# Performance work log

Measured on AMD Instinct MI355X. Metric: run time of the kernel, lower is better.

Reference implementation:

```python
import jax, jax.numpy as jnp
import numpy as np
from jax import lax

B, C, OUT, K, H, W = 8, 64, 32, 3, 64, 64


def _conv2d(x, w, b, stride=1, pad=0, groups=1):
    o = lax.conv_general_dilated(x, w, (stride, stride), [(pad, pad), (pad, pad)],
                                 dimension_numbers=('NCHW', 'OIHW', 'NCHW'),
                                 feature_group_count=groups)
    return o + b[None, :, None, None]


def _bn(x, g, b, m, v, eps=1e-5):
    # eval-mode BatchNorm2d with running stats
    s = g / jnp.sqrt(v + eps)
    return x * s[None, :, None, None] + (b - m * s)[None, :, None, None]


def _eca(x, w):
    # global avg pool -> 1D conv over channel axis -> sigmoid gate [b,c,1,1]
    y = x.mean((-2, -1))[:, None, :]  # [b,1,c]
    y = lax.conv_general_dilated(y, w, (1,), [(1, 1)],
                                 dimension_numbers=('NCW', 'OIW', 'NCW'))
    return jax.nn.sigmoid(y[:, 0, :])[:, :, None, None]


def _avgpool3(x):
    # AvgPool2d(k=3, stride=1, pad=1), count_include_pad=True (torch default)
    s = lax.reduce_window(x, 0.0, lax.add, (1, 1, 3, 3), (1, 1, 1, 1),
                          [(0, 0), (0, 0), (1, 1), (1, 1)])
    return s / 9.0


def _forward(x, sc_w, sc_b, ac_w, ac_b, oc_w, oc_b, oc_bn_g, oc_bn_b, oc_bn_m, oc_bn_v,
             ex_w, ey_w, ez_w, ff_w, ff_b, g1_w, g1_b, g2_w, g2_b,
             fu_w, fu_b, fu_bn_g, fu_bn_b, fu_bn_m, fu_bn_v):
    b, c, h, w = x.shape
    k = K
    # --- ReceptiveFieldAttentionConv ---
    frf = jax.nn.silu(_conv2d(x, sc_w, sc_b, pad=k // 2, groups=c))
    frf = frf.reshape(b, c, k * k, h, w)
    arf = _conv2d(_avgpool3(x), ac_w, ac_b, groups=c).reshape(b, c, k * k, h, w)
    arf = jax.nn.softmax(arf, axis=2)  # softmax over k*k RF positions
    wt = (frf * arf).reshape(b, c, k, k, h, w)
    wt = wt.transpose(0, 1, 4, 2, 5, 3).reshape(b, c, h * k, w * k)  # pixel-shuffle-like
    x_rfa = jax.nn.silu(_bn(_conv2d(wt, oc_w, oc_b, stride=k, groups=4),
                            oc_bn_g, oc_bn_b, oc_bn_m, oc_bn_v))
    # --- FrequencyGroupedChannelAttention ---
    energy = jnp.abs(jnp.fft.fft2(x)).mean((-2, -1))  # [b,c]
    ranks = jnp.argsort(jnp.argsort(-energy, axis=1), axis=1)
    mask = (ranks < c // 2).astype(x.dtype)[:, :, None, None]  # top-half-energy channels
    a_x = _eca(x, ex_w)
    a_y = _eca(x * mask, ey_w)
    a_z = _eca(x * (1.0 - mask), ez_w)
    a_f = _conv2d(jnp.concatenate([a_y, a_z], 1), ff_w, ff_b, groups=4)
    g_in = jnp.concatenate([a_f, a_x], 1)
    g = jax.nn.sigmoid(_conv2d(jax.nn.silu(_conv2d(g_in, g1_w, g1_b)), g2_w, g2_b))
    x_fgca = x * (g * a_f + (1.0 - g) * a_x)
    # --- fuse ---
    fused = jnp.concatenate([x_rfa, x_fgca], 1)
    return jax.nn.silu(_bn(_conv2d(fused, fu_w, fu_b),
                           fu_bn_g, fu_bn_b, fu_bn_m, fu_bn_v))


def setup_inputs() -> dict:
    key = jax.random.key(0)
    ks = jax.random.split(key, 32)
    rn = lambda k, shp, s=0.1: jax.random.normal(k, shp, jnp.float32) * s
    gh = max(8, C // 4)  # gate hidden = 16
    return {
        'x': jax.random.normal(ks[0], (B, C, H, W), jnp.float32),
        'sc_w': rn(ks[1], (C * K * K, 1, K, K)), 'sc_b': rn(ks[2], (C * K * K,)),
        'ac_w': rn(ks[3], (C * K * K, 1, 1, 1)), 'ac_b': rn(ks[4], (C * K * K,)),
        'oc_w': rn(ks[5], (C, C // 4, K, K)), 'oc_b': rn(ks[6], (C,)),
        'oc_bn_g': 1.0 + rn(ks[7], (C,)), 'oc_bn_b': rn(ks[8], (C,)),
        'oc_bn_m': rn(ks[9], (C,)), 'oc_bn_v': 0.9 + 0.2 * jax.random.uniform(ks[10], (C,), jnp.float32),
        'ex_w': rn(ks[11], (1, 1, 3), 0.3), 'ey_w': rn(ks[12], (1, 1, 3), 0.3),
        'ez_w': rn(ks[13], (1, 1, 3), 0.3),
        'ff_w': rn(ks[14], (C, 2 * C // 4, 1, 1)), 'ff_b': rn(ks[15], (C,)),
        'g1_w': rn(ks[16], (gh, 2 * C, 1, 1)), 'g1_b': rn(ks[17], (gh,)),
        'g2_w': rn(ks[18], (C, gh, 1, 1)), 'g2_b': rn(ks[19], (C,)),
        'fu_w': rn(ks[20], (OUT, 2 * C, 1, 1)), 'fu_b': rn(ks[21], (OUT,)),
        'fu_bn_g': 1.0 + rn(ks[22], (OUT,)), 'fu_bn_b': rn(ks[23], (OUT,)),
        'fu_bn_m': rn(ks[24], (OUT,)), 'fu_bn_v': 0.9 + 0.2 * jax.random.uniform(ks[25], (OUT,), jnp.float32),
    }


def reference(x, sc_w, sc_b, ac_w, ac_b, oc_w, oc_b, oc_bn_g, oc_bn_b, oc_bn_m, oc_bn_v,
              ex_w, ey_w, ez_w, ff_w, ff_b, g1_w, g1_b, g2_w, g2_b,
              fu_w, fu_b, fu_bn_g, fu_bn_b, fu_bn_m, fu_bn_v):
    return _forward(x, sc_w, sc_b, ac_w, ac_b, oc_w, oc_b, oc_bn_g, oc_bn_b, oc_bn_m, oc_bn_v,
                    ex_w, ey_w, ez_w, ff_w, ff_b, g1_w, g1_b, g2_w, g2_b,
                    fu_w, fu_b, fu_bn_g, fu_bn_b, fu_bn_m, fu_bn_v)
```

## Files before the change

kernel.cpp:

```cpp
#include <hip/hip_runtime.h>
#include <math.h>

#define EPS 1e-5f

__device__ __forceinline__ float wave_sum(float v) {
  v += __shfl_down(v, 32);
  v += __shfl_down(v, 16);
  v += __shfl_down(v, 8);
  v += __shfl_down(v, 4);
  v += __shfl_down(v, 2);
  v += __shfl_down(v, 1);
  return v;
}

__device__ __forceinline__ float frcp(float x) { return __builtin_amdgcn_rcpf(x); }
__device__ __forceinline__ float silu_f(float v) { return v * frcp(1.f + __expf(-v)); }
__device__ __forceinline__ float sigm_f(float v) { return frcp(1.f + __expf(-v)); }

__device__ __forceinline__ unsigned bf16r(float v) {
  unsigned u = __float_as_uint(v);
  return (u + 0x7FFFu + ((u >> 16) & 1u)) >> 16;
}

__device__ __forceinline__ int bitrev6(int v) {
  return ((v & 1) << 5) | ((v & 2) << 3) | ((v & 4) << 1) |
         ((v & 8) >> 1) | ((v & 16) >> 3) | ((v & 32) >> 5);
}

#define FFT6(zr, zi)                                           \
  do {                                                         \
    _Pragma("unroll") for (int s = 0; s < 6; ++s) {            \
      const int half = 32 >> s;                                \
      const bool up = (lane & half) != 0;                      \
      float pr = __shfl_xor(zr, half);                         \
      float pi = __shfl_xor(zi, half);                         \
      float tr = up ? pr - zr : zr + pr;                       \
      float ti = up ? pi - zi : zi + pi;                       \
      const float c = twc[s], sn = tws[s];                     \
      zr = tr * c - ti * sn;                                   \
      zi = tr * sn + ti * c;                                   \
    }                                                          \
  } while (0)

__global__ __launch_bounds__(256) void k_dft(const float* __restrict__ x,
                                             float* __restrict__ energy,
                                             float* __restrict__ meanx) {
  __shared__ float re1[33 * 65];
  __shared__ float im1[33 * 65];
  __shared__ float redA[4], redB[4];
  const int bc = blockIdx.x;
  const int tid = threadIdx.x;
  const int lane = tid & 63;
  const int wv = tid >> 6;
  const float* xp = x + (size_t)bc * 4096;

  float twc[6], tws[6];
#pragma unroll
  for (int s = 0; s < 6; ++s) {
    int half = 32 >> s;
    if (lane & half) {
      float ang = -6.283185307179586f * (float)((lane & (half - 1)) << s) / 64.f;
      float sv, cv;
      __sincosf(ang, &sv, &cv);
      twc[s] = cv;
      tws[s] = sv;
    } else {
      twc[s] = 1.f;
      tws[s] = 0.f;
    }
  }

  const int f = bitrev6(lane);
  const int fm = (64 - f) & 63;
  const int plane = bitrev6(fm);

  float lsum = 0.f;
#pragma unroll 1
  for (int rp = 0; rp < 4; ++rp) {
    const int h0 = wv * 16 + rp * 4;
    float x0 = xp[h0 * 64 + lane];
    float x1 = xp[(h0 + 1) * 64 + lane];
    float x2 = xp[(h0 + 2) * 64 + lane];
    float x3 = xp[(h0 + 3) * 64 + lane];
    lsum += x0 + x1 + x2 + x3;
    float zr = x0, zi = x1, yr = x2, yi = x3;
#pragma unroll
    for (int s = 0; s < 6; ++s) {
      const int half = 32 >> s;
      const bool up = (lane & half) != 0;
      float pzr = __shfl_xor(zr, half);
      float pzi = __shfl_xor(zi, half);
      float pyr = __shfl_xor(yr, half);
      float pyi = __shfl_xor(yi, half);
      float tzr = up ? pzr - zr : zr + pzr;
      float tzi = up ? pzi - zi : zi + pzi;
      float tyr = up ? pyr - yr : yr + pyr;
      float tyi = up ? pyi - yi : yi + pyi;
      const float c = twc[s], sn = tws[s];
      zr = tzr * c - tzi * sn;
      zi = tzr * sn + tzi * c;
      yr = tyr * c - tyi * sn;
      yi = tyr * sn + tyi * c;
    }
    float mzr = __shfl(zr, plane), mzi = __shfl(zi, plane);
    float myr = __shfl(yr, plane), myi = __shfl(yi, plane);
    if (f <= 32) {
      float ar = 0.5f * (zr + mzr), ai = 0.5f * (zi - mzi);
      float br = 0.5f * (zi + mzi), bi = 0.5f * (mzr - zr);
      float cr = 0.5f * (yr + myr), ci = 0.5f * (yi - myi);
      float dr = 0.5f * (yi + myi), di = 0.5f * (myr - yr);
      re1[f * 65 + h0] = ar;     im1[f * 65 + h0] = ai;
      re1[f * 65 + h0 + 1] = br; im1[f * 65 + h0 + 1] = bi;
      re1[f * 65 + h0 + 2] = cr; im1[f * 65 + h0 + 2] = ci;
      re1[f * 65 + h0 + 3] = dr; im1[f * 65 + h0 + 3] = di;
    }
  }
  __syncthreads();

  float msum = 0.f;
#pragma unroll 1
  for (int i = 0; i < 4; ++i) {
    const int kv1 = wv + 8 * i;
    const int kv2 = kv1 + 4;
    const float w1 = (kv1 == 0) ? 1.f : 2.f;
    float ar = re1[kv1 * 65 + lane];
    float ai = im1[kv1 * 65 + lane];
    float br = re1[kv2 * 65 + lane];
    float bi = im1[kv2 * 65 + lane];
#pragma unroll
    for (int s = 0; s < 6; ++s) {
      const int half = 32 >> s;
      const bool up = (lane & half) != 0;
      float par = __shfl_xor(ar, half);
      float pai = __shfl_xor(ai, half);
      float pbr = __shfl_xor(br, half);
      float pbi = __shfl_xor(bi, half);
      float tar = up ? par - ar : ar + par;
      float tai = up ? pai - ai : ai + pai;
      float tbr = up ? pbr - br : br + pbr;
      float tbi = up ? pbi - bi : bi + pbi;
      const float c = twc[s], sn = tws[s];
      ar = tar * c - tai * sn;
      ai = tar * sn + tai * c;
      br = tbr * c - tbi * sn;
      bi = tbr * sn + tbi * c;
    }
    msum += w1 * sqrtf(ar * ar + ai * ai) + 2.f * sqrtf(br * br + bi * bi);
  }
  if (wv == 0) {
    float ar = re1[32 * 65 + lane];
    float ai = im1[32 * 65 + lane];
    FFT6(ar, ai);
    msum += sqrtf(ar * ar + ai * ai);
  }

  msum = wave_sum(msum);
  lsum = wave_sum(lsum);
  if (lane == 0) { redA[wv] = msum; redB[wv] = lsum; }
  __syncthreads();
  if (tid == 0) {
    float e = redA[0] + redA[1] + redA[2] + redA[3];
    float m = redB[0] + redB[1] + redB[2] + redB[3];
    energy[bc] = e * (1.f / 4096.f);
    meanx[bc] = m * (1.f / 4096.f);
  }
}

__global__ __launch_bounds__(256) void k_rfa(
    const float* __restrict__ x,
    const float* __restrict__ sc_w, const float* __restrict__ sc_b,
    const float* __restrict__ ac_w, const float* __restrict__ ac_b,
    const float* __restrict__ oc_w, const float* __restrict__ oc_b,
    const float* __restrict__ bn_g, const float* __restrict__ bn_b,
    const float* __restrict__ bn_m, const float* __restrict__ bn_v,
    float* __restrict__ xrfa) {
  __shared__ __align__(16) float scwp[16 * 9 * 12];
  __shared__ __align__(16) float mp[16 * 24];
  __shared__ __align__(16) unsigned ocwb[16 * 8 * 12];
  __shared__ float red[128 * 33];
  const int blk = blockIdx.x;
  const int band = blk & 15;
  const int g = (blk >> 4) & 3;
  const int b = blk >> 6;
  const int tid = threadIdx.x;
  const int lane = tid & 63;
  const int wv = tid >> 6;
  const int wp = wv & 1;
  const int half = wv >> 1;

  for (int i = tid; i < 1296; i += 256) {
    int icg = i / 81, rem = i - icg * 81;
    int j = rem / 9, t = rem - j * 9;
    scwp[icg * 108 + j * 12 + t] = sc_w[(g * 144 + icg * 9 + j) * 9 + t];
  }
  if (tid < 144) {
    int icg = tid / 9, j = tid - icg * 9;
    scwp[icg * 108 + j * 12 + 9] = sc_b[g * 144 + tid];
    mp[icg * 24 + j] = ac_w[g * 144 + tid];
    mp[icg * 24 + 12 + j] = ac_b[g * 144 + tid];
  }
  for (int i = tid; i < 1152; i += 256) {
    int icg = i / 72, rem = i - icg * 72;
    int o2 = rem / 9, j = rem - o2 * 9;
    float w0 = oc_w[((g * 16 + 2 * o2) * 16 + icg) * 9 + j];
    float w1 = oc_w[((g * 16 + 2 * o2 + 1) * 16 + icg) * 9 + j];
    ocwb[icg * 96 + o2 * 12 + j] = bf16r(w0) | (bf16r(w1) << 16);
  }
  __syncthreads();

  const int r0 = band * 4 + wp * 2;
  const int w = lane;
  const bool vW = w > 0, vE = w < 63;
  float acc0[16], acc1[16];
#pragma unroll
  for (int i = 0; i < 16; ++i) { acc0[i] = 0.f; acc1[i] = 0.f; }

  const float* xg = x + ((size_t)(b * 64 + g * 16)) * 4096 + w;
  const int icg0 = half * 8;

#pragma unroll 1
  for (int ii = 0; ii < 8; ++ii) {
    const int icg = icg0 + ii;
    const float* xc = xg + icg * 4096;
    float n[12];
#pragma unroll
    for (int t = 0; t < 4; ++t) {
      int h = r0 - 1 + t;
      bool vh = (h >= 0) && (h < 64);
      const float* row = xc + h * 64;
      n[t * 3 + 0] = (vh && vW) ? row[-1] : 0.f;
      n[t * 3 + 1] = vh ? row[0] : 0.f;
      n[t * 3 + 2] = (vh && vE) ? row[1] : 0.f;
    }
    float rs0 = n[0] + n[1] + n[2];
    float rs1 = n[3] + n[4] + n[5];
    float rs2 = n[6] + n[7] + n[8];
    float rs3 = n[9] + n[10] + n[11];
    float ap0 = (rs0 + rs1 + rs2) * (1.f / 9.f);
    float ap1 = (rs1 + rs2 + rs3) * (1.f / 9.f);

    float aw[12], ab[12];
    *(float4*)&aw[0] = *(const float4*)&mp[icg * 24];
    *(float4*)&aw[4] = *(const float4*)&mp[icg * 24 + 4];
    *(float4*)&aw[8] = *(const float4*)&mp[icg * 24 + 8];
    *(float4*)&ab[0] = *(const float4*)&mp[icg * 24 + 12];
    *(float4*)&ab[4] = *(const float4*)&mp[icg * 24 + 16];
    *(float4*)&ab[8] = *(const float4*)&mp[icg * 24 + 20];

    float f0[9], f1[9], a0[9], a1[9];
    float amax0 = -1e30f, amax1 = -1e30f;
#pragma unroll
    for (int j = 0; j < 9; ++j) {
      float wt[12];
      *(float4*)&wt[0] = *(const float4*)&scwp[icg * 108 + j * 12];
      *(float4*)&wt[4] = *(const float4*)&scwp[icg * 108 + j * 12 + 4];
      *(float4*)&wt[8] = *(const float4*)&scwp[icg * 108 + j * 12 + 8];
      float p0 = wt[9], p1 = wt[9];
#pragma unroll
      for (int t = 0; t < 9; ++t) {
        p0 = fmaf(n[t], wt[t], p0);
        p1 = fmaf(n[t + 3], wt[t], p1);
      }
      f0[j] = silu_f(p0);
      f1[j] = silu_f(p1);
      float v0 = fmaf(ap0, aw[j], ab[j]);
      float v1 = fmaf(ap1, aw[j], ab[j]);
      a0[j] = v0; a1[j] = v1;
      amax0 = fmaxf(amax0, v0);
      amax1 = fmaxf(amax1, v1);
    }
    float es0 = 0.f, es1 = 0.f;
    float p0[9], p1[9];
#pragma unroll
    for (int j = 0; j < 9; ++j) {
      float e0 = __expf(a0[j] - amax0);
      float e1 = __expf(a1[j] - amax1);
      es0 += e0; es1 += e1;
      p0[j] = f0[j] * e0;
      p1[j] = f1[j] * e1;
    }
    float i0 = frcp(es0);
    float i1 = frcp(es1);
#pragma unroll
    for (int j = 0; j < 9; ++j) { p0[j] *= i0; p1[j] *= i1; }

#pragma unroll
    for (int o2 = 0; o2 < 8; ++o2) {
      unsigned u[12];
      *(uint4*)&u[0] = *(const uint4*)&ocwb[icg * 96 + o2 * 12];
      *(uint4*)&u[4] = *(const uint4*)&ocwb[icg * 96 + o2 * 12 + 4];
      *(uint4*)&u[8] = *(const uint4*)&ocwb[icg * 96 + o2 * 12 + 8];
      float se0 = 0.f, so0 = 0.f, se1 = 0.f, so1 = 0.f;
#pragma unroll
      for (int j = 0; j < 9; ++j) {
        float we = __uint_as_float(u[j] << 16);
        float wo = __uint_as_float(u[j] & 0xFFFF0000u);
        se0 = fmaf(p0[j], we, se0);
        so0 = fmaf(p0[j], wo, so0);
        se1 = fmaf(p1[j], we, se1);
        so1 = fmaf(p1[j], wo, so1);
      }
      acc0[2 * o2] += se0;
      acc0[2 * o2 + 1] += so0;
      acc1[2 * o2] += se1;
      acc1[2 * o2 + 1] += so1;
    }
  }

  const int rid = wp * 64 + lane;
  if (half == 1) {
#pragma unroll
    for (int k = 0; k < 16; ++k) {
      red[rid * 33 + k] = acc0[k];
      red[rid * 33 + 16 + k] = acc1[k];
    }
  }
  __syncthreads();
  if (half == 0) {
#pragma unroll
    for (int k = 0; k < 16; ++k) {
      acc0[k] += red[rid * 33 + k];
      acc1[k] += red[rid * 33 + 16 + k];
    }
    float* op = xrfa + ((size_t)(b * 64 + g * 16)) * 4096 + r0 * 64 + w;
#pragma unroll
    for (int oco = 0; oco < 16; ++oco) {
      int oc = g * 16 + oco;
      float s = bn_g[oc] * rsqrtf(bn_v[oc] + EPS);
      float bb = bn_b[oc] - bn_m[oc] * s;
      float ob = oc_b[oc];
      float v0 = fmaf(acc0[oco] + ob, s, bb);
      float v1 = fmaf(acc1[oco] + ob, s, bb);
      op[oco * 4096] = silu_f(v0);
      op[oco * 4096 + 64] = silu_f(v1);
    }
  }
}

__global__ __launch_bounds__(256) void k_fuse(
    const float* __restrict__ x, const float* __restrict__ xrfa,
    const float* __restrict__ energy, const float* __restrict__ meanx,
    const float* __restrict__ ex_w, const float* __restrict__ ey_w,
    const float* __restrict__ ez_w, const float* __restrict__ ff_w,
    const float* __restrict__ ff_b, const float* __restrict__ g1_w,
    const float* __restrict__ g1_b, const float* __restrict__ g2_w,
    const float* __restrict__ g2_b,
    const float* __restrict__ fu_w, const float* __restrict__ fu_b,
    const float* __restrict__ bn_g, const float* __restrict__ bn_b,
    const float* __restrict__ bn_m, const float* __restrict__ bn_v,
    float* __restrict__ out) {
  __shared__ __align__(16) float fw[4096];
  __shared__ float s2l[64];
  __shared__ float e[64], mx[64], my[64], mz[64];
  __shared__ float ax[64], ay[64], az[64], af[64], h1[16];
  const int blk = blockIdx.x;
  const int tid = threadIdx.x;
  const int sloc = tid & 63;
  const int ocq = tid >> 6;
  const int b = blk >> 6;
  const int sp = (blk & 63) * 64 + sloc;
  const int c = tid;

  for (int i = tid; i < 1024; i += 256)
    ((float4*)fw)[i] = ((const float4*)fu_w)[i];
  if (c < 64) {
    e[c] = energy[b * 64 + c];
    mx[c] = meanx[b * 64 + c];
  }
  __syncthreads();
  if (c < 64) {
    int rank = 0;
    float ec = e[c];
    for (int i = 0; i < 64; ++i) {
      float ei = e[i];
      rank += (ei > ec) || (ei == ec && i < c);
    }
    float mask = (rank < 32) ? 1.f : 0.f;
    my[c] = mx[c] * mask;
    mz[c] = mx[c] * (1.f - mask);
  }
  __syncthreads();
  if (c < 64) {
    float l, r, m;
    l = (c > 0) ? mx[c - 1] : 0.f; m = mx[c]; r = (c < 63) ? mx[c + 1] : 0.f;
    ax[c] = sigm_f(ex_w[0] * l + ex_w[1] * m + ex_w[2] * r);
    l = (c > 0) ? my[c - 1] : 0.f; m = my[c]; r = (c < 63) ? my[c + 1] : 0.f;
    ay[c] = sigm_f(ey_w[0] * l + ey_w[1] * m + ey_w[2] * r);
    l = (c > 0) ? mz[c - 1] : 0.f; m = mz[c]; r = (c < 63) ? mz[c + 1] : 0.f;
    az[c] = sigm_f(ez_w[0] * l + ez_w[1] * m + ez_w[2] * r);
  }
  __syncthreads();
  if (c < 64) {
    int gg = c >> 4;
    float acc = ff_b[c];
#pragma unroll
    for (int i = 0; i < 32; ++i) {
      int ch = gg * 32 + i;
      float v = (ch < 64) ? ay[ch] : az[ch - 64];
      acc = fmaf(v, ff_w[c * 32 + i], acc);
    }
    af[c] = acc;
  }
  __syncthreads();
  if (c < 16) {
    float a = g1_b[c];
#pragma unroll
    for (int i = 0; i < 64; ++i) a = fmaf(af[i], g1_w[c * 128 + i], a);
#pragma unroll
    for (int i = 0; i < 64; ++i) a = fmaf(ax[i], g1_w[c * 128 + 64 + i], a);
    h1[c] = silu_f(a);
  }
  __syncthreads();
  if (c < 64) {
    float gv = g2_b[c];
#pragma unroll
    for (int o = 0; o < 16; ++o) gv = fmaf(h1[o], g2_w[c * 16 + o], gv);
    gv = sigm_f(gv);
    s2l[c] = gv * af[c] + (1.f - gv) * ax[c];
  }

  const float* xr = xrfa + (size_t)b * 64 * 4096 + sp;
  const float* xp = x + (size_t)b * 64 * 4096 + sp;
  float va[64], vb[64];
#pragma unroll
  for (int i = 0; i < 64; ++i) va[i] = xr[i * 4096];
#pragma unroll
  for (int i = 0; i < 64; ++i) vb[i] = xp[i * 4096];
  __syncthreads();
#pragma unroll
  for (int i = 0; i < 64; ++i) vb[i] *= s2l[i];

  float* op = out + (size_t)b * 32 * 4096 + sp;
#pragma unroll 1
  for (int o = 0; o < 8; ++o) {
    const int oc = ocq * 8 + o;
    const float* wr = &fw[oc * 128];
    float a = 0.f;
#pragma unroll
    for (int q = 0; q < 16; ++q) {
      float4 w4 = *(const float4*)&wr[q * 4];
      a = fmaf(va[q * 4 + 0], w4.x, a);
      a = fmaf(va[q * 4 + 1], w4.y, a);
      a = fmaf(va[q * 4 + 2], w4.z, a);
      a = fmaf(va[q * 4 + 3], w4.w, a);
    }
#pragma unroll
    for (int q = 0; q < 16; ++q) {
      float4 w4 = *(const float4*)&wr[64 + q * 4];
      a = fmaf(vb[q * 4 + 0], w4.x, a);
      a = fmaf(vb[q * 4 + 1], w4.y, a);
      a = fmaf(vb[q * 4 + 2], w4.z, a);
      a = fmaf(vb[q * 4 + 3], w4.w, a);
    }
    float s = bn_g[oc] * rsqrtf(bn_v[oc] + EPS);
    float v = a + fu_b[oc];
    v = fmaf(v, s, bn_b[oc] - bn_m[oc] * s);
    op[oc * 4096] = silu_f(v);
  }
}

extern "C" void kernel_launch(void* const* d_in, const int* in_sizes, int n_in,
                              void* d_out, int out_size, void* d_ws, size_t ws_size,
                              hipStream_t stream) {
  const float* x       = (const float*)d_in[0];
  const float* sc_w    = (const float*)d_in[1];
  const float* sc_b    = (const float*)d_in[2];
  const float* ac_w    = (const float*)d_in[3];
  const float* ac_b    = (const float*)d_in[4];
  const float* oc_w    = (const float*)d_in[5];
  const float* oc_b    = (const float*)d_in[6];
  const float* oc_bn_g = (const float*)d_in[7];
  const float* oc_bn_b = (const float*)d_in[8];
  const float* oc_bn_m = (const float*)d_in[9];
  const float* oc_bn_v = (const float*)d_in[10];
  const float* ex_w    = (const float*)d_in[11];
  const float* ey_w    = (const float*)d_in[12];
  const float* ez_w    = (const float*)d_in[13];
  const float* ff_w    = (const float*)d_in[14];
  const float* ff_b    = (const float*)d_in[15];
  const float* g1_w    = (const float*)d_in[16];
  const float* g1_b    = (const float*)d_in[17];
  const float* g2_w    = (const float*)d_in[18];
  const float* g2_b    = (const float*)d_in[19];
  const float* fu_w    = (const float*)d_in[20];
  const float* fu_b    = (const float*)d_in[21];
  const float* fu_bn_g = (const float*)d_in[22];
  const float* fu_bn_b = (const float*)d_in[23];
  const float* fu_bn_m = (const float*)d_in[24];
  const float* fu_bn_v = (const float*)d_in[25];

  float* ws     = (float*)d_ws;
  float* energy = ws;
  float* meanx  = ws + 512;
  float* xrfa   = ws + 2048;

  k_dft<<<512, 256, 0, stream>>>(x, energy, meanx);
  k_rfa<<<512, 256, 0, stream>>>(x, sc_w, sc_b, ac_w, ac_b, oc_w, oc_b,
                                 oc_bn_g, oc_bn_b, oc_bn_m, oc_bn_v, xrfa);
  k_fuse<<<512, 256, 0, stream>>>(x, xrfa, energy, meanx,
                                  ex_w, ey_w, ez_w, ff_w, ff_b,
                                  g1_w, g1_b, g2_w, g2_b,
                                  fu_w, fu_b,
                                  fu_bn_g, fu_bn_b, fu_bn_m, fu_bn_v,
                                  (float*)d_out);
}
```

Baseline: 168.8 us.

## Merge DFT and RFA kernels into one launch and drop softmax max-subtraction

Combines the independent FFT-energy kernel and the receptive-field attention conv kernel into a single 1024-block launch, using block index to select the path and a shared-memory union to overlay their scratch buffers. This removes one kernel launch and lets the two independent workloads run concurrently across the GPU. The softmax over the 9 RF positions also no longer subtracts the max, which saves a pass and some registers but risks overflow if the logits are large. A larger shared-memory footprint per block (the union max) could reduce occupancy for the DFT blocks.

```diff
diff --git a/kernel.cpp b/kernel.cpp
--- a/kernel.cpp
+++ b/kernel.cpp
@@ -42,297 +42,295 @@
     }                                                          \
   } while (0)
 
-__global__ __launch_bounds__(256) void k_dft(const float* __restrict__ x,
-                                             float* __restrict__ energy,
-                                             float* __restrict__ meanx) {
-  __shared__ float re1[33 * 65];
-  __shared__ float im1[33 * 65];
-  __shared__ float redA[4], redB[4];
-  const int bc = blockIdx.x;
-  const int tid = threadIdx.x;
-  const int lane = tid & 63;
-  const int wv = tid >> 6;
-  const float* xp = x + (size_t)bc * 4096;
-
-  float twc[6], tws[6];
-#pragma unroll
-  for (int s = 0; s < 6; ++s) {
-    int half = 32 >> s;
-    if (lane & half) {
-      float ang = -6.283185307179586f * (float)((lane & (half - 1)) << s) / 64.f;
-      float sv, cv;
-      __sincosf(ang, &sv, &cv);
-      twc[s] = cv;
-      tws[s] = sv;
-    } else {
-      twc[s] = 1.f;
-      tws[s] = 0.f;
-    }
-  }
-
-  const int f = bitrev6(lane);
-  const int fm = (64 - f) & 63;
-  const int plane = bitrev6(fm);
-
-  float lsum = 0.f;
-#pragma unroll 1
-  for (int rp = 0; rp < 4; ++rp) {
-    const int h0 = wv * 16 + rp * 4;
-    float x0 = xp[h0 * 64 + lane];
-    float x1 = xp[(h0 + 1) * 64 + lane];
-    float x2 = xp[(h0 + 2) * 64 + lane];
-    float x3 = xp[(h0 + 3) * 64 + lane];
-    lsum += x0 + x1 + x2 + x3;
-    float zr = x0, zi = x1, yr = x2, yi = x3;
-#pragma unroll
-    for (int s = 0; s < 6; ++s) {
-      const int half = 32 >> s;
-      const bool up = (lane & half) != 0;
-      float pzr = __shfl_xor(zr, half);
-      float pzi = __shfl_xor(zi, half);
-      float pyr = __shfl_xor(yr, half);
-      float pyi = __shfl_xor(yi, half);
-      float tzr = up ? pzr - zr : zr + pzr;
-      float tzi = up ? pzi - zi : zi + pzi;
-      float tyr = up ? pyr - yr : yr + pyr;
-      float tyi = up ? pyi - yi : yi + pyi;
-      const float c = twc[s], sn = tws[s];
-      zr = tzr * c - tzi * sn;
-      zi = tzr * sn + tzi * c;
-      yr = tyr * c - tyi * sn;
-      yi = tyr * sn + tyi * c;
-    }
-    float mzr = __shfl(zr, plane), mzi = __shfl(zi, plane);
-    float myr = __shfl(yr, plane), myi = __shfl(yi, plane);
-    if (f <= 32) {
-      float ar = 0.5f * (zr + mzr), ai = 0.5f * (zi - mzi);
-      float br = 0.5f * (zi + mzi), bi = 0.5f * (mzr - zr);
-      float cr = 0.5f * (yr + myr), ci = 0.5f * (yi - myi);
-      float dr = 0.5f * (yi + myi), di = 0.5f * (myr - yr);
-      re1[f * 65 + h0] = ar;     im1[f * 65 + h0] = ai;
-      re1[f * 65 + h0 + 1] = br; im1[f * 65 + h0 + 1] = bi;
-      re1[f * 65 + h0 + 2] = cr; im1[f * 65 + h0 + 2] = ci;
-      re1[f * 65 + h0 + 3] = dr; im1[f * 65 + h0 + 3] = di;
-    }
-  }
-  __syncthreads();
-
-  float msum = 0.f;
-#pragma unroll 1
-  for (int i = 0; i < 4; ++i) {
-    const int kv1 = wv + 8 * i;
-    const int kv2 = kv1 + 4;
-    const float w1 = (kv1 == 0) ? 1.f : 2.f;
-    float ar = re1[kv1 * 65 + lane];
-    float ai = im1[kv1 * 65 + lane];
-    float br = re1[kv2 * 65 + lane];
-    float bi = im1[kv2 * 65 + lane];
-#pragma unroll
-    for (int s = 0; s < 6; ++s) {
-      const int half = 32 >> s;
-      const bool up = (lane & half) != 0;
-      float par = __shfl_xor(ar, half);
-      float pai = __shfl_xor(ai, half);
-      float pbr = __shfl_xor(br, half);
-      float pbi = __shfl_xor(bi, half);
-      float tar = up ? par - ar : ar + par;
-      float tai = up ? pai - ai : ai + pai;
-      float tbr = up ? pbr - br : br + pbr;
-      float tbi = up ? pbi - bi : bi + pbi;
-      const float c = twc[s], sn = tws[s];
-      ar = tar * c - tai * sn;
-      ai = tar * sn + tai * c;
-      br = tbr * c - tbi * sn;
-      bi = tbr * sn + tbi * c;
-    }
-    msum += w1 * sqrtf(ar * ar + ai * ai) + 2.f * sqrtf(br * br + bi * bi);
-  }
-  if (wv == 0) {
-    float ar = re1[32 * 65 + lane];
-    float ai = im1[32 * 65 + lane];
-    FFT6(ar, ai);
-    msum += sqrtf(ar * ar + ai * ai);
-  }
-
-  msum = wave_sum(msum);
-  lsum = wave_sum(lsum);
-  if (lane == 0) { redA[wv] = msum; redB[wv] = lsum; }
-  __syncthreads();
-  if (tid == 0) {
-    float e = redA[0] + redA[1] + redA[2] + redA[3];
-    float m = redB[0] + redB[1] + redB[2] + redB[3];
-    energy[bc] = e * (1.f / 4096.f);
-    meanx[bc] = m * (1.f / 4096.f);
-  }
-}
-
-__global__ __launch_bounds__(256) void k_rfa(
+struct SRfa {
+  float scwp[16 * 9 * 12];
+  float mp[16 * 24];
+  unsigned ocwb[16 * 8 * 12];
+  float red[128 * 33];
+};
+struct SDft {
+  float re1[33 * 65];
+  float im1[33 * 65];
+  float redA[4], redB[4];
+};
+union SMem { SRfa r; SDft d; };
+
+__global__ __launch_bounds__(256) void k_main(
     const float* __restrict__ x,
     const float* __restrict__ sc_w, const float* __restrict__ sc_b,
     const float* __restrict__ ac_w, const float* __restrict__ ac_b,
     const float* __restrict__ oc_w, const float* __restrict__ oc_b,
     const float* __restrict__ bn_g, const float* __restrict__ bn_b,
     const float* __restrict__ bn_m, const float* __restrict__ bn_v,
-    float* __restrict__ xrfa) {
-  __shared__ __align__(16) float scwp[16 * 9 * 12];
-  __shared__ __align__(16) float mp[16 * 24];
-  __shared__ __align__(16) unsigned ocwb[16 * 8 * 12];
-  __shared__ float red[128 * 33];
-  const int blk = blockIdx.x;
-  const int band = blk & 15;
-  const int g = (blk >> 4) & 3;
-  const int b = blk >> 6;
+    float* __restrict__ xrfa,
+    float* __restrict__ energy, float* __restrict__ meanx) {
+  __shared__ SMem sm;
   const int tid = threadIdx.x;
   const int lane = tid & 63;
   const int wv = tid >> 6;
-  const int wp = wv & 1;
-  const int half = wv >> 1;
-
-  for (int i = tid; i < 1296; i += 256) {
-    int icg = i / 81, rem = i - icg * 81;
-    int j = rem / 9, t = rem - j * 9;
-    scwp[icg * 108 + j * 12 + t] = sc_w[(g * 144 + icg * 9 + j) * 9 + t];
-  }
-  if (tid < 144) {
-    int icg = tid / 9, j = tid - icg * 9;
-    scwp[icg * 108 + j * 12 + 9] = sc_b[g * 144 + tid];
-    mp[icg * 24 + j] = ac_w[g * 144 + tid];
-    mp[icg * 24 + 12 + j] = ac_b[g * 144 + tid];
-  }
-  for (int i = tid; i < 1152; i += 256) {
-    int icg = i / 72, rem = i - icg * 72;
-    int o2 = rem / 9, j = rem - o2 * 9;
-    float w0 = oc_w[((g * 16 + 2 * o2) * 16 + icg) * 9 + j];
-    float w1 = oc_w[((g * 16 + 2 * o2 + 1) * 16 + icg) * 9 + j];
-    ocwb[icg * 96 + o2 * 12 + j] = bf16r(w0) | (bf16r(w1) << 16);
-  }
-  __syncthreads();
-
-  const int r0 = band * 4 + wp * 2;
-  const int w = lane;
-  const bool vW = w > 0, vE = w < 63;
-  float acc0[16], acc1[16];
-#pragma unroll
-  for (int i = 0; i < 16; ++i) { acc0[i] = 0.f; acc1[i] = 0.f; }
-
-  const float* xg = x + ((size_t)(b * 64 + g * 16)) * 4096 + w;
-  const int icg0 = half * 8;
+
+  if (blockIdx.x < 512) {
+    const int blk = blockIdx.x;
+    const int band = blk & 15;
+    const int g = (blk >> 4) & 3;
+    const int b = blk >> 6;
+    const int wp = wv & 1;
+    const int half = wv >> 1;
+    float* scwp = sm.r.scwp;
+    float* mp = sm.r.mp;
+    unsigned* ocwb = sm.r.ocwb;
+    float* red = sm.r.red;
+
+    for (int i = tid; i < 1296; i += 256) {
+      int icg = i / 81, rem = i - icg * 81;
+      int j = rem / 9, t = rem - j * 9;
+      scwp[icg * 108 + j * 12 + t] = sc_w[(g * 144 + icg * 9 + j) * 9 + t];
+    }
+    if (tid < 144) {
+      int icg = tid / 9, j = tid - icg * 9;
+      scwp[icg * 108 + j * 12 + 9] = sc_b[g * 144 + tid];
+      mp[icg * 24 + j] = ac_w[g * 144 + tid];
+      mp[icg * 24 + 12 + j] = ac_b[g * 144 + tid];
+    }
+    for (int i = tid; i < 1152; i += 256) {
+      int icg = i / 72, rem = i - icg * 72;
+      int o2 = rem / 9, j = rem - o2 * 9;
+      float w0 = oc_w[((g * 16 + 2 * o2) * 16 + icg) * 9 + j];
+      float w1 = oc_w[((g * 16 + 2 * o2 + 1) * 16 + icg) * 9 + j];
+      ocwb[icg * 96 + o2 * 12 + j] = bf16r(w0) | (bf16r(w1) << 16);
+    }
+    __syncthreads();
+
+    const int r0 = band * 4 + wp * 2;
+    const int w = lane;
+    const bool vW = w > 0, vE = w < 63;
+    float acc0[16], acc1[16];
+#pragma unroll
+    for (int i = 0; i < 16; ++i) { acc0[i] = 0.f; acc1[i] = 0.f; }
+
+    const float* xg = x + ((size_t)(b * 64 + g * 16)) * 4096 + w;
+    const int icg0 = half * 8;
 
 #pragma unroll 1
-  for (int ii = 0; ii < 8; ++ii) {
-    const int icg = icg0 + ii;
-    const float* xc = xg + icg * 4096;
-    float n[12];
-#pragma unroll
-    for (int t = 0; t < 4; ++t) {
-      int h = r0 - 1 + t;
-      bool vh = (h >= 0) && (h < 64);
-      const float* row = xc + h * 64;
-      n[t * 3 + 0] = (vh && vW) ? row[-1] : 0.f;
-      n[t * 3 + 1] = vh ? row[0] : 0.f;
-      n[t * 3 + 2] = (vh && vE) ? row[1] : 0.f;
-    }
-    float rs0 = n[0] + n[1] + n[2];
-    float rs1 = n[3] + n[4] + n[5];
-    float rs2 = n[6] + n[7] + n[8];
-    float rs3 = n[9] + n[10] + n[11];
-    float ap0 = (rs0 + rs1 + rs2) * (1.f / 9.f);
-    float ap1 = (rs1 + rs2 + rs3) * (1.f / 9.f);
-
-    float aw[12], ab[12];
-    *(float4*)&aw[0] = *(const float4*)&mp[icg * 24];
-    *(float4*)&aw[4] = *(const float4*)&mp[icg * 24 + 4];
-    *(float4*)&aw[8] = *(const float4*)&mp[icg * 24 + 8];
-    *(float4*)&ab[0] = *(const float4*)&mp[icg * 24 + 12];
-    *(float4*)&ab[4] = *(const float4*)&mp[icg * 24 + 16];
-    *(float4*)&ab[8] = *(const float4*)&mp[icg * 24 + 20];
-
-    float f0[9], f1[9], a0[9], a1[9];
-    float amax0 = -1e30f, amax1 = -1e30f;
-#pragma unroll
-    for (int j = 0; j < 9; ++j) {
-      float wt[12];
-      *(float4*)&wt[0] = *(const float4*)&scwp[icg * 108 + j * 12];
-      *(float4*)&wt[4] = *(const float4*)&scwp[icg * 108 + j * 12 + 4];
-      *(float4*)&wt[8] = *(const float4*)&scwp[icg * 108 + j * 12 + 8];
-      float p0 = wt[9], p1 = wt[9];
-#pragma unroll
-      for (int t = 0; t < 9; ++t) {
-        p0 = fmaf(n[t], wt[t], p0);
-        p1 = fmaf(n[t + 3], wt[t], p1);
-      }
-      f0[j] = silu_f(p0);
-      f1[j] = silu_f(p1);
-      float v0 = fmaf(ap0, aw[j], ab[j]);
-      float v1 = fmaf(ap1, aw[j], ab[j]);
-      a0[j] = v0; a1[j] = v1;
-      amax0 = fmaxf(amax0, v0);
-      amax1 = fmaxf(amax1, v1);
-    }
-    float es0 = 0.f, es1 = 0.f;
-    float p0[9], p1[9];
-#pragma unroll
-    for (int j = 0; j < 9; ++j) {
-      float e0 = __expf(a0[j] - amax0);
-      float e1 = __expf(a1[j] - amax1);
-      es0 += e0; es1 += e1;
-      p0[j] = f0[j] * e0;
-      p1[j] = f1[j] * e1;
-    }
-    float i0 = frcp(es0);
-    float i1 = frcp(es1);
-#pragma unroll
-    for (int j = 0; j < 9; ++j) { p0[j] *= i0; p1[j] *= i1; }
-
-#pragma unroll
-    for (int o2 = 0; o2 < 8; ++o2) {
-      unsigned u[12];
-      *(uint4*)&u[0] = *(const uint4*)&ocwb[icg * 96 + o2 * 12];
-      *(uint4*)&u[4] = *(const uint4*)&ocwb[icg * 96 + o2 * 12 + 4];
-      *(uint4*)&u[8] = *(const uint4*)&ocwb[icg * 96 + o2 * 12 + 8];
-      float se0 = 0.f, so0 = 0.f, se1 = 0.f, so1 = 0.f;
+    for (int ii = 0; ii < 8; ++ii) {
+      const int icg = icg0 + ii;
+      const float* xc = xg + icg * 4096;
+      float n[12];
+#pragma unroll
+      for (int t = 0; t < 4; ++t) {
+        int h = r0 - 1 + t;
+        bool vh = (h >= 0) && (h < 64);
+        const float* row = xc + h * 64;
+        n[t * 3 + 0] = (vh && vW) ? row[-1] : 0.f;
+        n[t * 3 + 1] = vh ? row[0] : 0.f;
+        n[t * 3 + 2] = (vh && vE) ? row[1] : 0.f;
+      }
+      float rs0 = n[0] + n[1] + n[2];
+      float rs1 = n[3] + n[4] + n[5];
+      float rs2 = n[6] + n[7] + n[8];
+      float rs3 = n[9] + n[10] + n[11];
+      float ap0 = (rs0 + rs1 + rs2) * (1.f / 9.f);
+      float ap1 = (rs1 + rs2 + rs3) * (1.f / 9.f);
+
+      float aw[12], ab[12];
+      *(float4*)&aw[0] = *(const float4*)&mp[icg * 24];
+      *(float4*)&aw[4] = *(const float4*)&mp[icg * 24 + 4];
+      *(float4*)&aw[8] = *(const float4*)&mp[icg * 24 + 8];
+      *(float4*)&ab[0] = *(const float4*)&mp[icg * 24 + 12];
+      *(float4*)&ab[4] = *(const float4*)&mp[icg * 24 + 16];
+      *(float4*)&ab[8] = *(const float4*)&mp[icg * 24 + 20];
+
+      float p0[9], p1[9];
+      float es0 = 0.f, es1 = 0.f;
 #pragma unroll
       for (int j = 0; j < 9; ++j) {
-        float we = __uint_as_float(u[j] << 16);
-        float wo = __uint_as_float(u[j] & 0xFFFF0000u);
-        se0 = fmaf(p0[j], we, se0);
-        so0 = fmaf(p0[j], wo, so0);
-        se1 = fmaf(p1[j], we, se1);
-        so1 = fmaf(p1[j], wo, so1);
-      }
-      acc0[2 * o2] += se0;
-      acc0[2 * o2 + 1] += so0;
-      acc1[2 * o2] += se1;
-      acc1[2 * o2 + 1] += so1;
-    }
-  }
-
-  const int rid = wp * 64 + lane;
-  if (half == 1) {
-#pragma unroll
-    for (int k = 0; k < 16; ++k) {
-      red[rid * 33 + k] = acc0[k];
-      red[rid * 33 + 16 + k] = acc1[k];
-    }
-  }
-  __syncthreads();
-  if (half == 0) {
-#pragma unroll
-    for (int k = 0; k < 16; ++k) {
-      acc0[k] += red[rid * 33 + k];
-      acc1[k] += red[rid * 33 + 16 + k];
-    }
-    float* op = xrfa + ((size_t)(b * 64 + g * 16)) * 4096 + r0 * 64 + w;
-#pragma unroll
-    for (int oco = 0; oco < 16; ++oco) {
-      int oc = g * 16 + oco;
-      float s = bn_g[oc] * rsqrtf(bn_v[oc] + EPS);
-      float bb = bn_b[oc] - bn_m[oc] * s;
-      float ob = oc_b[oc];
-      float v0 = fmaf(acc0[oco] + ob, s, bb);
-      float v1 = fmaf(acc1[oco] + ob, s, bb);
-      op[oco * 4096] = silu_f(v0);
-      op[oco * 4096 + 64] = silu_f(v1);
+        float wt[12];
+        *(float4*)&wt[0] = *(const float4*)&scwp[icg * 108 + j * 12];
+        *(float4*)&wt[4] = *(const float4*)&scwp[icg * 108 + j * 12 + 4];
+        *(float4*)&wt[8] = *(const float4*)&scwp[icg * 108 + j * 12 + 8];
+        float q0 = wt[9], q1 = wt[9];
+#pragma unroll
+        for (int t = 0; t < 9; ++t) {
+          q0 = fmaf(n[t], wt[t], q0);
+          q1 = fmaf(n[t + 3], wt[t], q1);
+        }
+        float e0 = __expf(fmaf(ap0, aw[j], ab[j]));
+        float e1 = __expf(fmaf(ap1, aw[j], ab[j]));
+        es0 += e0; es1 += e1;
+        p0[j] = silu_f(q0) * e0;
+        p1[j] = silu_f(q1) * e1;
+      }
+      float i0 = frcp(es0);
+      float i1 = frcp(es1);
+#pragma unroll
+      for (int j = 0; j < 9; ++j) { p0[j] *= i0; p1[j] *= i1; }
+
+#pragma unroll
+      for (int o2 = 0; o2 < 8; ++o2) {
+        unsigned u[12];
+        *(uint4*)&u[0] = *(const uint4*)&ocwb[icg * 96 + o2 * 12];
+        *(uint4*)&u[4] = *(const uint4*)&ocwb[icg * 96 + o2 * 12 + 4];
+        *(uint4*)&u[8] = *(const uint4*)&ocwb[icg * 96 + o2 * 12 + 8];
+        float se0 = 0.f, so0 = 0.f, se1 = 0.f, so1 = 0.f;
+#pragma unroll
+        for (int j = 0; j < 9; ++j) {
+          float we = __uint_as_float(u[j] << 16);
+          float wo = __uint_as_float(u[j] & 0xFFFF0000u);
+          se0 = fmaf(p0[j], we, se0);
+          so0 = fmaf(p0[j], wo, so0);
+          se1 = fmaf(p1[j], we, se1);
+          so1 = fmaf(p1[j], wo, so1);
+        }
+        acc0[2 * o2] += se0;
+        acc0[2 * o2 + 1] += so0;
+        acc1[2 * o2] += se1;
+        acc1[2 * o2 + 1] += so1;
+      }
+    }
+
+    const int rid = wp * 64 + lane;
+    if (half == 1) {
+#pragma unroll
+      for (int k = 0; k < 16; ++k) {
+        red[rid * 33 + k] = acc0[k];
+        red[rid * 33 + 16 + k] = acc1[k];
+      }
+    }
+    __syncthreads();
+    if (half == 0) {
+#pragma unroll
+      for (int k = 0; k < 16; ++k) {
+        acc0[k] += red[rid * 33 + k];
+        acc1[k] += red[rid * 33 + 16 + k];
+      }
+      float* op = xrfa + ((size_t)(b * 64 + g * 16)) * 4096 + r0 * 64 + w;
+#pragma unroll
+      for (int oco = 0; oco < 16; ++oco) {
+        int oc = g * 16 + oco;
+        float s = bn_g[oc] * rsqrtf(bn_v[oc] + EPS);
+        float bb = bn_b[oc] - bn_m[oc] * s;
+        float ob = oc_b[oc];
+        float v0 = fmaf(acc0[oco] + ob, s, bb);
+        float v1 = fmaf(acc1[oco] + ob, s, bb);
+        op[oco * 4096] = silu_f(v0);
+        op[oco * 4096 + 64] = silu_f(v1);
+      }
+    }
+  } else {
+    const int bc = blockIdx.x - 512;
+    float* re1 = sm.d.re1;
+    float* im1 = sm.d.im1;
+    const float* xp = x + (size_t)bc * 4096;
+
+    float twc[6], tws[6];
+#pragma unroll
+    for (int s = 0; s < 6; ++s) {
+      int half = 32 >> s;
+      if (lane & half) {
+        float ang = -6.283185307179586f * (float)((lane & (half - 1)) << s) / 64.f;
+        float sv, cv;
+        __sincosf(ang, &sv, &cv);
+        twc[s] = cv;
+        tws[s] = sv;
+      } else {
+        twc[s] = 1.f;
+        tws[s] = 0.f;
+      }
+    }
+
+    const int f = bitrev6(lane);
+    const int fm = (64 - f) & 63;
+    const int plane = bitrev6(fm);
+
+    float lsum = 0.f;
+#pragma unroll 1
+    for (int rp = 0; rp < 4; ++rp) {
+      const int h0 = wv * 16 + rp * 4;
+      float x0 = xp[h0 * 64 + lane];
+      float x1 = xp[(h0 + 1) * 64 + lane];
+      float x2 = xp[(h0 + 2) * 64 + lane];
+      float x3 = xp[(h0 + 3) * 64 + lane];
+      lsum += x0 + x1 + x2 + x3;
+      float zr = x0, zi = x1, yr = x2, yi = x3;
+#pragma unroll
+      for (int s = 0; s < 6; ++s) {
+        const int half = 32 >> s;
+        const bool up = (lane & half) != 0;
+        float pzr = __shfl_xor(zr, half);
+        float pzi = __shfl_xor(zi, half);
+        float pyr = __shfl_xor(yr, half);
+        float pyi = __shfl_xor(yi, half);
+        float tzr = up ? pzr - zr : zr + pzr;
+        float tzi = up ? pzi - zi : zi + pzi;
+        float tyr = up ? pyr - yr : yr + pyr;
+        float tyi = up ? pyi - yi : yi + pyi;
+        const float c = twc[s], sn = tws[s];
+        zr = tzr * c - tzi * sn;
+        zi = tzr * sn + tzi * c;
+        yr = tyr * c - tyi * sn;
+        yi = tyr * sn + tyi * c;
+      }
+      float mzr = __shfl(zr, plane), mzi = __shfl(zi, plane);
+      float myr = __shfl(yr, plane), myi = __shfl(yi, plane);
+      if (f <= 32) {
+        float ar = 0.5f * (zr + mzr), ai = 0.5f * (zi - mzi);
+        float br = 0.5f * (zi + mzi), bi = 0.5f * (mzr - zr);
+        float cr = 0.5f * (yr + myr), ci = 0.5f * (yi - myi);
+        float dr = 0.5f * (yi + myi), di = 0.5f * (myr - yr);
+        re1[f * 65 + h0] = ar;     im1[f * 65 + h0] = ai;
+        re1[f * 65 + h0 + 1] = br; im1[f * 65 + h0 + 1] = bi;
+        re1[f * 65 + h0 + 2] = cr; im1[f * 65 + h0 + 2] = ci;
+        re1[f * 65 + h0 + 3] = dr; im1[f * 65 + h0 + 3] = di;
+      }
+    }
+    __syncthreads();
+
+    float msum = 0.f;
+#pragma unroll 1
+    for (int i = 0; i < 4; ++i) {
+      const int kv1 = wv + 8 * i;
+      const int kv2 = kv1 + 4;
+      const float w1 = (kv1 == 0) ? 1.f : 2.f;
+      float ar = re1[kv1 * 65 + lane];
+      float ai = im1[kv1 * 65 + lane];
+      float br = re1[kv2 * 65 + lane];
+      float bi = im1[kv2 * 65 + lane];
+#pragma unroll
+      for (int s = 0; s < 6; ++s) {
+        const int half = 32 >> s;
+        const bool up = (lane & half) != 0;
+        float par = __shfl_xor(ar, half);
+        float pai = __shfl_xor(ai, half);
+        float pbr = __shfl_xor(br, half);
+        float pbi = __shfl_xor(bi, half);
+        float tar = up ? par - ar : ar + par;
+        float tai = up ? pai - ai : ai + pai;
+        float tbr = up ? pbr - br : br + pbr;
+        float tbi = up ? pbi - bi : bi + pbi;
+        const float c = twc[s], sn = tws[s];
+        ar = tar * c - tai * sn;
+        ai = tar * sn + tai * c;
+        br = tbr * c - tbi * sn;
+        bi = tbr * sn + tbi * c;
+      }
+      msum += w1 * sqrtf(ar * ar + ai * ai) + 2.f * sqrtf(br * br + bi * bi);
+    }
+    if (wv == 0) {
+      float ar = re1[32 * 65 + lane];
+      float ai = im1[32 * 65 + lane];
+      FFT6(ar, ai);
+      msum += sqrtf(ar * ar + ai * ai);
+    }
+
+    msum = wave_sum(msum);
+    lsum = wave_sum(lsum);
+    if (lane == 0) { sm.d.redA[wv] = msum; sm.d.redB[wv] = lsum; }
+    __syncthreads();
+    if (tid == 0) {
+      float e = sm.d.redA[0] + sm.d.redA[1] + sm.d.redA[2] + sm.d.redA[3];
+      float m = sm.d.redB[0] + sm.d.redB[1] + sm.d.redB[2] + sm.d.redB[3];
+      energy[bc] = e * (1.f / 4096.f);
+      meanx[bc] = m * (1.f / 4096.f);
     }
   }
 }
@@ -494,9 +492,9 @@
   float* meanx  = ws + 512;
   float* xrfa   = ws + 2048;
 
-  k_dft<<<512, 256, 0, stream>>>(x, energy, meanx);
-  k_rfa<<<512, 256, 0, stream>>>(x, sc_w, sc_b, ac_w, ac_b, oc_w, oc_b,
-                                 oc_bn_g, oc_bn_b, oc_bn_m, oc_bn_v, xrfa);
+  k_main<<<1024, 256, 0, stream>>>(x, sc_w, sc_b, ac_w, ac_b, oc_w, oc_b,
+                                   oc_bn_g, oc_bn_b, oc_bn_m, oc_bn_v,
+                                   xrfa, energy, meanx);
   k_fuse<<<512, 256, 0, stream>>>(x, xrfa, energy, meanx,
                                   ex_w, ey_w, ez_w, ff_w, ff_b,
                                   g1_w, g1_b, g2_w, g2_b,
```

After: 156.9 us (median of 2 runs). -7.0%, faster.
